# Performance work log

Measured on AMD Instinct MI355X. Metric: run time of the kernel, lower is better.

## Reference

```python
import jax, jax.numpy as jnp
import numpy as np
from jax import lax

T, D_IN, N = 8192, 1024, 1024


def setup_inputs() -> dict:
    key = jax.random.key(0)
    ks = jax.random.split(key, 8)
    s = 0.1  # truncated_normal stddev in original
    return {
        "x": jax.random.normal(ks[0], (T, D_IN), jnp.float32),
        # input projections (FullConnectLayer weights + biases)
        "Wx": jax.random.normal(ks[1], (D_IN, N), jnp.float32) * s,
        "bx": jnp.zeros((N,), jnp.float32),
        "Wu": jax.random.normal(ks[2], (D_IN, N), jnp.float32) * s,
        "bu": jnp.zeros((N,), jnp.float32),
        "Wr": jax.random.normal(ks[3], (D_IN, N), jnp.float32) * s,
        "br": jnp.zeros((N,), jnp.float32),
        # recurrent weights/biases
        "hW": jax.random.normal(ks[4], (N, N), jnp.float32) * s,
        "hUW": jax.random.normal(ks[5], (N, N), jnp.float32) * s,
        "hRW": jax.random.normal(ks[6], (N, N), jnp.float32) * s,
        "hB": jnp.zeros((N,), jnp.float32),
        "hUB": jnp.zeros((N,), jnp.float32),
        "hRB": jnp.zeros((N,), jnp.float32),
        # initial hidden state h (tf.Variable zeros [1, nNodes])
        "h0": jnp.zeros((1, N), jnp.float32),
    }


def reference(x, Wx, bx, Wu, bu, Wr, br, hW, hUW, hRW, hB, hUB, hRB, h0):
    # Precompute input-side gate projections for all timesteps (as original
    # does: xTransform/xUpdates/xResets are built once on the full sequence).
    xT = x @ Wx + bx  # [T, N] candidate input
    xU = x @ Wu + bu  # [T, N] update gate input
    xR = x @ Wr + br  # [T, N] reset gate input

    def step(h, xs):  # h: [N]
        xt, xu, xr = xs
        u = jax.nn.sigmoid(xu + h @ hUW + hUB)
        r = jax.nn.sigmoid(xr + h @ hRW + hRB)
        hc = jnp.tanh(xt + (r * h) @ hW + hB)
        # NOTE: faithful to original bug: (1-u)*hc + u*hc == hc
        h_new = (1.0 - u) * hc + u * hc
        return h_new, h_new

    _, hs = lax.scan(step, h0[0], (xT, xU, xR))
    return hs  # [T, N] == hStates.concat() since each state is [1, N]
```

## Files before the change

kernel.cpp:

```cpp
#include <hip/hip_runtime.h>
#include <hip/hip_bf16.h>
#include <math.h>

#define T_STEPS 8192
#define NN      1024
#define KWG     32
#define WCOLS   32
#define RTHREADS 512

__global__ __launch_bounds__(256) void gemm_bias(
    const float* __restrict__ A, const float* __restrict__ W,
    const float* __restrict__ bias, float* __restrict__ C)
{
    const int bn = blockIdx.x;
    const int bm = blockIdx.y;
    const int tid = threadIdx.x;

    __shared__ float As[16][64];
    __shared__ float Bs[16][64];

    const int row0 = bm * 64, col0 = bn * 64;
    const int tm = (tid >> 4) << 2;
    const int tn = (tid & 15) << 2;

    float acc[4][4] = {};

    for (int k0 = 0; k0 < 1024; k0 += 16) {
        {
            const int m = tid >> 2, kq = (tid & 3) << 2;
            const float4 v = *reinterpret_cast<const float4*>(&A[(size_t)(row0 + m) * 1024 + k0 + kq]);
            As[kq + 0][m] = v.x; As[kq + 1][m] = v.y; As[kq + 2][m] = v.z; As[kq + 3][m] = v.w;
            const int kk = tid >> 4, nq = (tid & 15) << 2;
            *reinterpret_cast<float4*>(&Bs[kk][nq]) =
                *reinterpret_cast<const float4*>(&W[(size_t)(k0 + kk) * 1024 + col0 + nq]);
        }
        __syncthreads();
#pragma unroll
        for (int k = 0; k < 16; ++k) {
            const float4 a4 = *reinterpret_cast<const float4*>(&As[k][tm]);
            const float4 b4 = *reinterpret_cast<const float4*>(&Bs[k][tn]);
            const float a[4] = {a4.x, a4.y, a4.z, a4.w};
            const float b[4] = {b4.x, b4.y, b4.z, b4.w};
#pragma unroll
            for (int i = 0; i < 4; ++i)
#pragma unroll
                for (int j = 0; j < 4; ++j) acc[i][j] += a[i] * b[j];
        }
        __syncthreads();
    }
#pragma unroll
    for (int i = 0; i < 4; ++i)
#pragma unroll
        for (int j = 0; j < 4; ++j)
            C[(size_t)(row0 + tm + i) * 1024 + col0 + tn + j] = acc[i][j] + bias[col0 + tn + j];
}

__global__ __launch_bounds__(RTHREADS, 2) void gru_rec(
    const float* __restrict__ xT, const float* __restrict__ xR,
    const float* __restrict__ hRW, const float* __restrict__ hW,
    const float* __restrict__ hRB, const float* __restrict__ hB,
    const float* __restrict__ h0, float* __restrict__ out,
    float* __restrict__ slots,
    unsigned int* __restrict__ flags)
{
    const int g = blockIdx.x;
    const int tid = threadIdx.x;
    const int lane = tid & 63;
    const int wave = tid >> 6;

    __shared__ float hsh[NN];
    __shared__ float part[16][WCOLS];
    __shared__ float rh[WCOLS];

    const int j1 = tid & (WCOLS - 1);
    const int sub = tid >> 5;
    float w1[64];
#pragma unroll
    for (int k = 0; k < 64; ++k)
        w1[k] = hRW[(size_t)(sub * 64 + k) * NN + g * WCOLS + j1];

    const int n0 = tid, n1 = tid + RTHREADS;
    float w2a[32], w2b[32];
#pragma unroll
    for (int k = 0; k < 32; ++k) {
        w2a[k] = hW[(size_t)(g * WCOLS + k) * NN + n0];
        w2b[k] = hW[(size_t)(g * WCOLS + k) * NN + n1];
    }

    const float hB0 = hB[n0], hB1 = hB[n1];
    float hRBj = 0.f;
    if (wave == 0 && lane < WCOLS) hRBj = hRB[g * WCOLS + lane];

    hsh[n0] = h0[n0];
    hsh[n1] = h0[n1];
    __syncthreads();

    for (int t = 0; t < T_STEPS; ++t) {
        const float xt0 = xT[(size_t)t * NN + n0];
        const float xt1 = xT[(size_t)t * NN + n1];
        const float xr = (wave == 0 && lane < WCOLS) ? xR[(size_t)t * NN + g * WCOLS + lane] : 0.f;

        float a0 = 0.f, a1 = 0.f, a2 = 0.f, a3 = 0.f;
#pragma unroll
        for (int k = 0; k < 64; k += 4) {
            const float4 hv = *reinterpret_cast<const float4*>(&hsh[sub * 64 + k]);
            a0 += hv.x * w1[k + 0];
            a1 += hv.y * w1[k + 1];
            a2 += hv.z * w1[k + 2];
            a3 += hv.w * w1[k + 3];
        }
        part[sub][j1] = (a0 + a1) + (a2 + a3);
        __syncthreads();

        if (wave == 0) {
            const int jj = lane & 31;
            const int sh = lane >> 5;
            float s = 0.f;
#pragma unroll
            for (int q = 0; q < 8; ++q) s += part[sh * 8 + q][jj];
            s += __shfl_xor(s, 32);
            if (lane < WCOLS) {
                const float z = xr + hRBj + s;
                const float r = 1.f / (1.f + expf(-z));
                rh[lane] = r * hsh[g * WCOLS + lane];
            }
        }
        __syncthreads();

        float b0 = 0.f, b1 = 0.f, c0 = 0.f, c1 = 0.f;
#pragma unroll
        for (int k = 0; k < 32; k += 2) {
            const float2 rv = *reinterpret_cast<const float2*>(&rh[k]);
            b0 += rv.x * w2a[k];  b1 += rv.y * w2a[k + 1];
            c0 += rv.x * w2b[k];  c1 += rv.y * w2b[k + 1];
        }
        const float p0 = b0 + b1, p1 = c0 + c1;

        float* slot = slots + ((size_t)(t & 1) * KWG + g) * NN;
        __hip_atomic_store(&slot[n0], p0, __ATOMIC_RELAXED, __HIP_MEMORY_SCOPE_AGENT);
        __hip_atomic_store(&slot[n1], p1, __ATOMIC_RELAXED, __HIP_MEMORY_SCOPE_AGENT);
        __syncthreads();

        if (tid == 0)
            __hip_atomic_store(&flags[g * 16], (unsigned)(t + 1),
                               __ATOMIC_RELEASE, __HIP_MEMORY_SCOPE_AGENT);

        if (wave == 0 && lane < KWG) {
            while (__hip_atomic_load(&flags[lane * 16], __ATOMIC_RELAXED,
                                     __HIP_MEMORY_SCOPE_AGENT) <= (unsigned)t) {}
        }
        __syncthreads();

        const float* sl = slots + (size_t)(t & 1) * KWG * NN;
        float s0 = 0.f, s1 = 0.f;
#pragma unroll
        for (int gg = 0; gg < KWG; ++gg) {
            s0 += __hip_atomic_load(&sl[gg * NN + n0], __ATOMIC_RELAXED, __HIP_MEMORY_SCOPE_AGENT);
            s1 += __hip_atomic_load(&sl[gg * NN + n1], __ATOMIC_RELAXED, __HIP_MEMORY_SCOPE_AGENT);
        }
        const float h0n = tanhf(xt0 + s0 + hB0);
        const float h1n = tanhf(xt1 + s1 + hB1);
        hsh[n0] = h0n;
        hsh[n1] = h1n;
        if ((n0 >> 5) == g) out[(size_t)t * NN + n0] = h0n;
        if ((n1 >> 5) == g) out[(size_t)t * NN + n1] = h1n;
        __syncthreads();
    }
}

extern "C" void kernel_launch(void* const* d_in, const int* in_sizes, int n_in,
                              void* d_out, int out_size, void* d_ws, size_t ws_size,
                              hipStream_t stream) {
    const float* x   = (const float*)d_in[0];
    const float* Wx  = (const float*)d_in[1];
    const float* bx  = (const float*)d_in[2];
    const float* Wr  = (const float*)d_in[5];
    const float* br  = (const float*)d_in[6];
    const float* hW  = (const float*)d_in[7];
    const float* hRW = (const float*)d_in[9];
    const float* hB  = (const float*)d_in[10];
    const float* hRB = (const float*)d_in[12];
    const float* h0  = (const float*)d_in[13];
    float* out = (float*)d_out;

    char* ws = (char*)d_ws;
    float* xT = (float*)(ws);
    float* xR = (float*)(ws + 33554432);
    float* slots = (float*)(ws + 67108864);
    unsigned int* flags = (unsigned int*)(ws + 67108864 + 262144);

    hipMemsetAsync(flags, 0, KWG * 16 * sizeof(unsigned int), stream);

    gemm_bias<<<dim3(16, 128), 256, 0, stream>>>(x, Wx, bx, xT);
    gemm_bias<<<dim3(16, 128), 256, 0, stream>>>(x, Wr, br, xR);

    gru_rec<<<dim3(KWG), RTHREADS, 0, stream>>>(xT, xR, hRW, hW, hRB, hB, h0,
                                                out, slots, flags);
}
```

Measured before the change: 33.74 ms.

## Replace flag barrier with fixed-point atomic-add accumulation slots and shuffle reductions

```diff
diff --git a/kernel.cpp b/kernel.cpp
--- a/kernel.cpp
+++ b/kernel.cpp
@@ -5,8 +5,17 @@
 #define T_STEPS 8192
 #define NN      1024
 #define KWG     32
-#define WCOLS   32
-#define RTHREADS 512
+#define RT      512
+
+__device__ __forceinline__ float fast_sigmoid(float z) {
+    z = fminf(fmaxf(z, -30.f), 30.f);
+    return 1.f / (1.f + __expf(-z));
+}
+__device__ __forceinline__ float fast_tanh(float x) {
+    x = fminf(fmaxf(x, -9.f), 9.f);
+    const float e = __expf(2.f * x);
+    return (e - 1.f) / (e + 1.f);
+}
 
 __global__ __launch_bounds__(256) void gemm_bias(
     const float* __restrict__ A, const float* __restrict__ W,
@@ -16,8 +25,8 @@
     const int bm = blockIdx.y;
     const int tid = threadIdx.x;
 
-    __shared__ float As[16][64];
-    __shared__ float Bs[16][64];
+    __shared__ __align__(16) float As[16][68];
+    __shared__ __align__(16) float Bs[16][68];
 
     const int row0 = bm * 64, col0 = bn * 64;
     const int tm = (tid >> 4) << 2;
@@ -55,117 +64,113 @@
             C[(size_t)(row0 + tm + i) * 1024 + col0 + tn + j] = acc[i][j] + bias[col0 + tn + j];
 }
 
-__global__ __launch_bounds__(RTHREADS, 2) void gru_rec(
+__global__ __launch_bounds__(RT, 2) void gru_rec(
     const float* __restrict__ xT, const float* __restrict__ xR,
     const float* __restrict__ hRW, const float* __restrict__ hW,
     const float* __restrict__ hRB, const float* __restrict__ hB,
     const float* __restrict__ h0, float* __restrict__ out,
-    float* __restrict__ slots,
-    unsigned int* __restrict__ flags)
+    unsigned long long* __restrict__ slots)
 {
     const int g = blockIdx.x;
     const int tid = threadIdx.x;
     const int lane = tid & 63;
     const int wave = tid >> 6;
 
-    __shared__ float hsh[NN];
-    __shared__ float part[16][WCOLS];
-    __shared__ float rh[WCOLS];
-
-    const int j1 = tid & (WCOLS - 1);
-    const int sub = tid >> 5;
+    __shared__ __align__(16) float hsh[1088];
+    __shared__ __align__(16) float rh[32];
+
+    const int j = (wave << 2) | (lane >> 4);
+    const int c = lane & 15;
+    const bool leader = (c == 0);
+
     float w1[64];
 #pragma unroll
     for (int k = 0; k < 64; ++k)
-        w1[k] = hRW[(size_t)(sub * 64 + k) * NN + g * WCOLS + j1];
-
-    const int n0 = tid, n1 = tid + RTHREADS;
+        w1[k] = hRW[(size_t)(c * 64 + k) * NN + g * 32 + j];
+
+    const int n0 = tid, n1 = tid + RT;
+    const int pi0 = n0 + (n0 >> 6) * 4, pi1 = n1 + (n1 >> 6) * 4;
     float w2a[32], w2b[32];
 #pragma unroll
     for (int k = 0; k < 32; ++k) {
-        w2a[k] = hW[(size_t)(g * WCOLS + k) * NN + n0];
-        w2b[k] = hW[(size_t)(g * WCOLS + k) * NN + n1];
+        w2a[k] = hW[(size_t)(g * 32 + k) * NN + n0];
+        w2b[k] = hW[(size_t)(g * 32 + k) * NN + n1];
     }
-
     const float hB0 = hB[n0], hB1 = hB[n1];
-    float hRBj = 0.f;
-    if (wave == 0 && lane < WCOLS) hRBj = hRB[g * WCOLS + lane];
-
-    hsh[n0] = h0[n0];
-    hsh[n1] = h0[n1];
+    const int mj = g * 32 + j;
+    const int pij = mj + (mj >> 6) * 4;
+    const float hRBj = leader ? hRB[mj] : 0.f;
+    const bool own0 = ((n0 >> 5) == g), own1 = ((n1 >> 5) == g);
+
+    hsh[pi0] = h0[n0];
+    hsh[pi1] = h0[n1];
     __syncthreads();
 
-    for (int t = 0; t < T_STEPS; ++t) {
-        const float xt0 = xT[(size_t)t * NN + n0];
-        const float xt1 = xT[(size_t)t * NN + n1];
-        const float xr = (wave == 0 && lane < WCOLS) ? xR[(size_t)t * NN + g * WCOLS + lane] : 0.f;
-
-        float a0 = 0.f, a1 = 0.f, a2 = 0.f, a3 = 0.f;
-#pragma unroll
-        for (int k = 0; k < 64; k += 4) {
-            const float4 hv = *reinterpret_cast<const float4*>(&hsh[sub * 64 + k]);
-            a0 += hv.x * w1[k + 0];
-            a1 += hv.y * w1[k + 1];
-            a2 += hv.z * w1[k + 2];
-            a3 += hv.w * w1[k + 3];
-        }
-        part[sub][j1] = (a0 + a1) + (a2 + a3);
-        __syncthreads();
-
-        if (wave == 0) {
-            const int jj = lane & 31;
-            const int sh = lane >> 5;
-            float s = 0.f;
-#pragma unroll
-            for (int q = 0; q < 8; ++q) s += part[sh * 8 + q][jj];
-            s += __shfl_xor(s, 32);
-            if (lane < WCOLS) {
-                const float z = xr + hRBj + s;
-                const float r = 1.f / (1.f + expf(-z));
-                rh[lane] = r * hsh[g * WCOLS + lane];
-            }
-        }
-        __syncthreads();
-
-        float b0 = 0.f, b1 = 0.f, c0 = 0.f, c1 = 0.f;
-#pragma unroll
-        for (int k = 0; k < 32; k += 2) {
-            const float2 rv = *reinterpret_cast<const float2*>(&rh[k]);
-            b0 += rv.x * w2a[k];  b1 += rv.y * w2a[k + 1];
-            c0 += rv.x * w2b[k];  c1 += rv.y * w2b[k + 1];
-        }
-        const float p0 = b0 + b1, p1 = c0 + c1;
-
-        float* slot = slots + ((size_t)(t & 1) * KWG + g) * NN;
-        __hip_atomic_store(&slot[n0], p0, __ATOMIC_RELAXED, __HIP_MEMORY_SCOPE_AGENT);
-        __hip_atomic_store(&slot[n1], p1, __ATOMIC_RELAXED, __HIP_MEMORY_SCOPE_AGENT);
-        __syncthreads();
-
-        if (tid == 0)
-            __hip_atomic_store(&flags[g * 16], (unsigned)(t + 1),
-                               __ATOMIC_RELEASE, __HIP_MEMORY_SCOPE_AGENT);
-
-        if (wave == 0 && lane < KWG) {
-            while (__hip_atomic_load(&flags[lane * 16], __ATOMIC_RELAXED,
-                                     __HIP_MEMORY_SCOPE_AGENT) <= (unsigned)t) {}
-        }
-        __syncthreads();
-
-        const float* sl = slots + (size_t)(t & 1) * KWG * NN;
-        float s0 = 0.f, s1 = 0.f;
-#pragma unroll
-        for (int gg = 0; gg < KWG; ++gg) {
-            s0 += __hip_atomic_load(&sl[gg * NN + n0], __ATOMIC_RELAXED, __HIP_MEMORY_SCOPE_AGENT);
-            s1 += __hip_atomic_load(&sl[gg * NN + n1], __ATOMIC_RELAXED, __HIP_MEMORY_SCOPE_AGENT);
-        }
-        const float h0n = tanhf(xt0 + s0 + hB0);
-        const float h1n = tanhf(xt1 + s1 + hB1);
-        hsh[n0] = h0n;
-        hsh[n1] = h1n;
-        if ((n0 >> 5) == g) out[(size_t)t * NN + n0] = h0n;
-        if ((n1 >> 5) == g) out[(size_t)t * NN + n1] = h1n;
-        __syncthreads();
+    float hp0 = 0.f, hp1 = 0.f;
+    unsigned long long pA0 = 0, pA1 = 0, pB0 = 0, pB1 = 0;
+    unsigned long long tgA = 0, tgB = 0;
+    const float SC = 1048576.f, ISC = 1.f / 1048576.f;
+
+#define GRU_STEP(T_, SL_, PV0_, PV1_, TG_) do { \
+    const float xt0 = xT[(size_t)(T_) * NN + n0]; \
+    const float xt1 = xT[(size_t)(T_) * NN + n1]; \
+    float xr = 0.f; \
+    if (leader) xr = xR[(size_t)(T_) * NN + mj]; \
+    if ((T_) > 0) {   \
+        if (own0) out[(size_t)((T_) - 1) * NN + n0] = hp0; \
+        if (own1) out[(size_t)((T_) - 1) * NN + n1] = hp1; \
+    } \
+    float a0 = 0.f, a1 = 0.f, a2 = 0.f, a3 = 0.f; \
+    _Pragma("unroll") \
+    for (int k = 0; k < 64; k += 4) { \
+        const float4 hv = *reinterpret_cast<const float4*>(&hsh[c * 68 + k]); \
+        a0 += hv.x * w1[k + 0]; a1 += hv.y * w1[k + 1]; \
+        a2 += hv.z * w1[k + 2]; a3 += hv.w * w1[k + 3]; \
+    } \
+    float s = (a0 + a1) + (a2 + a3); \
+    s += __shfl_xor(s, 1); s += __shfl_xor(s, 2); \
+    s += __shfl_xor(s, 4); s += __shfl_xor(s, 8); \
+    if (leader) rh[j] = fast_sigmoid(xr + hRBj + s) * hsh[pij]; \
+    __syncthreads(); \
+    float b0 = 0.f, b1 = 0.f, d0 = 0.f, d1 = 0.f; \
+    _Pragma("unroll") \
+    for (int k = 0; k < 32; k += 2) { \
+        const float2 rv = *reinterpret_cast<const float2*>(&rh[k]); \
+        b0 += rv.x * w2a[k]; b1 += rv.y * w2a[k + 1]; \
+        d0 += rv.x * w2b[k]; d1 += rv.y * w2b[k + 1]; \
+    } \
+    const unsigned long long q0 = (1ULL << 38) + \
+        (unsigned long long)(long long)llrintf((b0 + b1) * SC); \
+    const unsigned long long q1 = (1ULL << 38) + \
+        (unsigned long long)(long long)llrintf((d0 + d1) * SC); \
+    __hip_atomic_fetch_add(&(SL_)[n0], q0, __ATOMIC_RELAXED, __HIP_MEMORY_SCOPE_AGENT); \
+    __hip_atomic_fetch_add(&(SL_)[n1], q1, __ATOMIC_RELAXED, __HIP_MEMORY_SCOPE_AGENT); \
+    TG_ += (unsigned long long)KWG << 38; \
+    const long long thr = (long long)TG_ - (1LL << 36); \
+    unsigned long long v0 = 0, v1 = 0; \
+    bool f0 = false, f1 = false; \
+    do { \
+        if (!f0) { v0 = __hip_atomic_load(&(SL_)[n0], __ATOMIC_RELAXED, __HIP_MEMORY_SCOPE_AGENT); \
+                   f0 = ((long long)v0 >= thr); } \
+        if (!f1) { v1 = __hip_atomic_load(&(SL_)[n1], __ATOMIC_RELAXED, __HIP_MEMORY_SCOPE_AGENT); \
+                   f1 = ((long long)v1 >= thr); } \
+    } while (!(f0 && f1)); \
+    const float s0 = (float)(long long)(v0 - PV0_ - ((unsigned long long)KWG << 38)) * ISC; \
+    const float s1 = (float)(long long)(v1 - PV1_ - ((unsigned long long)KWG << 38)) * ISC; \
+    PV0_ = v0; PV1_ = v1; \
+    hp0 = fast_tanh(xt0 + s0 + hB0); \
+    hp1 = fast_tanh(xt1 + s1 + hB1); \
+    hsh[pi0] = hp0; hsh[pi1] = hp1; \
+    __syncthreads(); \
+} while (0)
+
+    for (int t = 0; t < T_STEPS; t += 2) {
+        GRU_STEP(t,     slots,      pA0, pA1, tgA);
+        GRU_STEP(t + 1, slots + NN, pB0, pB1, tgB);
     }
+#undef GRU_STEP
+    if (own0) out[(size_t)(T_STEPS - 1) * NN + n0] = hp0;
+    if (own1) out[(size_t)(T_STEPS - 1) * NN + n1] = hp1;
 }
 
 extern "C" void kernel_launch(void* const* d_in, const int* in_sizes, int n_in,
@@ -186,14 +191,13 @@
     char* ws = (char*)d_ws;
     float* xT = (float*)(ws);
     float* xR = (float*)(ws + 33554432);
-    float* slots = (float*)(ws + 67108864);
-    unsigned int* flags = (unsigned int*)(ws + 67108864 + 262144);
-
-    hipMemsetAsync(flags, 0, KWG * 16 * sizeof(unsigned int), stream);
+    unsigned long long* slots = (unsigned long long*)(ws + 67108864);
+
+    hipMemsetAsync(slots, 0, 2 * NN * sizeof(unsigned long long), stream);
 
     gemm_bias<<<dim3(16, 128), 256, 0, stream>>>(x, Wx, bx, xT);
     gemm_bias<<<dim3(16, 128), 256, 0, stream>>>(x, Wr, br, xR);
 
-    gru_rec<<<dim3(KWG), RTHREADS, 0, stream>>>(xT, xR, hRW, hW, hRB, hB, h0,
-                                                out, slots, flags);
-}
+    gru_rec<<<dim3(KWG), RT, 0, stream>>>(xT, xR, hRW, hW, hRB, hB, h0,
+                                          out, slots);
+}
```

Measured after the change: 33.07 ms. -2.0%, faster.
